# Kernel optimization log

Measured on AMD Instinct MI355X. Metric: run time of the kernel, lower is better.

The kernel has to match this reference:

```python
import jax, jax.numpy as jnp
import numpy as np


def _skew(vec):
    # 3x3 skew-symmetric matrix of a 3-vector
    z = jnp.zeros((), dtype=vec.dtype)
    return jnp.array([[z, -vec[2], vec[1]],
                      [vec[2], z, -vec[0]],
                      [-vec[1], vec[0], z]])


def _exp_se3(w, v, theta):
    W = _skew(w)                      # 3x3
    W2 = W @ W
    s, c = jnp.sin(theta), jnp.cos(theta)
    I3 = jnp.eye(3, dtype=w.dtype)
    R = I3 + s * W + (1.0 - c) * W2                       # rotation block
    V = I3 * theta + (1.0 - c) * W + (theta - s) * W2     # left Jacobian-like
    t = V @ v                                              # translation
    top = jnp.concatenate([R, t[:, None]], axis=1)         # 3x4
    bottom = jnp.array([[0.0, 0.0, 0.0, 1.0]], dtype=w.dtype)
    return jnp.concatenate([top, bottom], axis=0)          # 4x4


def setup_inputs() -> dict:
    key = jax.random.key(0)
    k1, k2, k3, k4 = jax.random.split(key, 4)
    B = 4194304
    return {
        "w": jax.random.normal(k1, (3,), dtype=jnp.float32) * 1e-6,
        "v": jax.random.normal(k2, (3,), dtype=jnp.float32) * 1e-6,
        "theta": jax.random.normal(k3, (), dtype=jnp.float32) * 1e-6,
        "x": jax.random.normal(k4, (B, 4, 4), dtype=jnp.float32),
    }


def reference(w, v, theta, x):
    exp_i = _exp_se3(w, v, theta)              # 4x4
    return jnp.einsum('ij,bjk->bik', exp_i, x)  # broadcast matmul over batch
```

## Files before the change

### kernel.cpp

```cpp
#include <hip/hip_runtime.h>


__global__ __launch_bounds__(256) void se3_apply_kernel(
    const float* __restrict__ w3,
    const float* __restrict__ v3,
    const float* __restrict__ th1,
    const float* __restrict__ x,
    float* __restrict__ out,
    int B)
{
    const float wx = w3[0], wy = w3[1], wz = w3[2];
    const float vx = v3[0], vy = v3[1], vz = v3[2];
    const float th = th1[0];
    const float s = sinf(th);
    const float c = cosf(th);
    const float a = 1.0f - c;
    const float bq = th - s;

    const float W00 = 0.f,  W01 = -wz, W02 =  wy;
    const float W10 =  wz,  W11 = 0.f, W12 = -wx;
    const float W20 = -wy,  W21 =  wx, W22 = 0.f;

    const float Q00 = -(wy*wy + wz*wz), Q01 = wx*wy,            Q02 = wx*wz;
    const float Q10 = wx*wy,            Q11 = -(wx*wx + wz*wz), Q12 = wy*wz;
    const float Q20 = wx*wz,            Q21 = wy*wz,            Q22 = -(wx*wx + wy*wy);

    const float R00 = 1.0f + s*W00 + a*Q00;
    const float R01 =        s*W01 + a*Q01;
    const float R02 =        s*W02 + a*Q02;
    const float R10 =        s*W10 + a*Q10;
    const float R11 = 1.0f + s*W11 + a*Q11;
    const float R12 =        s*W12 + a*Q12;
    const float R20 =        s*W20 + a*Q20;
    const float R21 =        s*W21 + a*Q21;
    const float R22 = 1.0f + s*W22 + a*Q22;

    const float V00 = th   + a*W00 + bq*Q00;
    const float V01 =        a*W01 + bq*Q01;
    const float V02 =        a*W02 + bq*Q02;
    const float V10 =        a*W10 + bq*Q10;
    const float V11 = th   + a*W11 + bq*Q11;
    const float V12 =        a*W12 + bq*Q12;
    const float V20 =        a*W20 + bq*Q20;
    const float V21 =        a*W21 + bq*Q21;
    const float V22 = th   + a*W22 + bq*Q22;

    const float t0 = V00*vx + V01*vy + V02*vz;
    const float t1 = V10*vx + V11*vy + V12*vz;
    const float t2 = V20*vx + V21*vy + V22*vz;

    const int b = blockIdx.x * blockDim.x + threadIdx.x;
    if (b >= B) return;

    const float4* __restrict__ xv = reinterpret_cast<const float4*>(x) + (size_t)b * 4;
    float4* __restrict__ ov       = reinterpret_cast<float4*>(out)      + (size_t)b * 4;

    const float4 r0 = xv[0];
    const float4 r1 = xv[1];
    const float4 r2 = xv[2];
    const float4 r3 = xv[3];

    float4 o0, o1, o2;
    o0.x = R00*r0.x + R01*r1.x + R02*r2.x + t0*r3.x;
    o0.y = R00*r0.y + R01*r1.y + R02*r2.y + t0*r3.y;
    o0.z = R00*r0.z + R01*r1.z + R02*r2.z + t0*r3.z;
    o0.w = R00*r0.w + R01*r1.w + R02*r2.w + t0*r3.w;

    o1.x = R10*r0.x + R11*r1.x + R12*r2.x + t1*r3.x;
    o1.y = R10*r0.y + R11*r1.y + R12*r2.y + t1*r3.y;
    o1.z = R10*r0.z + R11*r1.z + R12*r2.z + t1*r3.z;
    o1.w = R10*r0.w + R11*r1.w + R12*r2.w + t1*r3.w;

    o2.x = R20*r0.x + R21*r1.x + R22*r2.x + t2*r3.x;
    o2.y = R20*r0.y + R21*r1.y + R22*r2.y + t2*r3.y;
    o2.z = R20*r0.z + R21*r1.z + R22*r2.z + t2*r3.z;
    o2.w = R20*r0.w + R21*r1.w + R22*r2.w + t2*r3.w;

    ov[0] = o0;
    ov[1] = o1;
    ov[2] = o2;
    ov[3] = r3;
}

extern "C" void kernel_launch(void* const* d_in, const int* in_sizes, int n_in,
                              void* d_out, int out_size, void* d_ws, size_t ws_size,
                              hipStream_t stream) {
    const float* w  = (const float*)d_in[0];
    const float* v  = (const float*)d_in[1];
    const float* th = (const float*)d_in[2];
    const float* x  = (const float*)d_in[3];
    float* out = (float*)d_out;

    const int B = in_sizes[3] / 16;
    const int block = 256;
    const int grid = (B + block - 1) / block;
    se3_apply_kernel<<<grid, block, 0, stream>>>(w, v, th, x, out, B);
}
```

Before: 448.4 us.

## Assign one output row per thread with cross-lane shuffles for matrix rows

Switches from one 4x4 matrix per thread (four strided float4 loads and stores) to one float4 row per thread, so consecutive lanes access consecutive 16-byte chunks and memory accesses are fully coalesced. Each thread gathers the four rows of its matrix from its 4-lane cluster via 16 shuffles and computes one output row with per-lane selected coefficients. This adds shuffle (LDS crossbar) traffic and launches four times as many threads, each recomputing the exp-map constants.

```diff
diff --git a/kernel.cpp b/kernel.cpp
--- a/kernel.cpp
+++ b/kernel.cpp
@@ -1,13 +1,13 @@
 #include <hip/hip_runtime.h>
 
 
-__global__ __launch_bounds__(256) void se3_apply_kernel(
+__global__ __launch_bounds__(256) void se3_apply_rows(
     const float* __restrict__ w3,
     const float* __restrict__ v3,
     const float* __restrict__ th1,
     const float* __restrict__ x,
     float* __restrict__ out,
-    int B)
+    int NR)
 {
     const float wx = w3[0], wy = w3[1], wz = w3[2];
     const float vx = v3[0], vy = v3[1], vz = v3[2];
@@ -17,69 +17,69 @@
     const float a = 1.0f - c;
     const float bq = th - s;
 
-    const float W00 = 0.f,  W01 = -wz, W02 =  wy;
-    const float W10 =  wz,  W11 = 0.f, W12 = -wx;
-    const float W20 = -wy,  W21 =  wx, W22 = 0.f;
+    const float W01 = -wz, W02 =  wy;
+    const float W10 =  wz, W12 = -wx;
+    const float W20 = -wy, W21 =  wx;
 
     const float Q00 = -(wy*wy + wz*wz), Q01 = wx*wy,            Q02 = wx*wz;
     const float Q10 = wx*wy,            Q11 = -(wx*wx + wz*wz), Q12 = wy*wz;
     const float Q20 = wx*wz,            Q21 = wy*wz,            Q22 = -(wx*wx + wy*wy);
 
-    const float R00 = 1.0f + s*W00 + a*Q00;
+    const float R00 = 1.0f + a*Q00;
     const float R01 =        s*W01 + a*Q01;
     const float R02 =        s*W02 + a*Q02;
     const float R10 =        s*W10 + a*Q10;
-    const float R11 = 1.0f + s*W11 + a*Q11;
+    const float R11 = 1.0f + a*Q11;
     const float R12 =        s*W12 + a*Q12;
     const float R20 =        s*W20 + a*Q20;
     const float R21 =        s*W21 + a*Q21;
-    const float R22 = 1.0f + s*W22 + a*Q22;
+    const float R22 = 1.0f + a*Q22;
 
-    const float V00 = th   + a*W00 + bq*Q00;
+    const float V00 = th   + bq*Q00;
     const float V01 =        a*W01 + bq*Q01;
     const float V02 =        a*W02 + bq*Q02;
     const float V10 =        a*W10 + bq*Q10;
-    const float V11 = th   + a*W11 + bq*Q11;
+    const float V11 = th   + bq*Q11;
     const float V12 =        a*W12 + bq*Q12;
     const float V20 =        a*W20 + bq*Q20;
     const float V21 =        a*W21 + bq*Q21;
-    const float V22 = th   + a*W22 + bq*Q22;
+    const float V22 = th   + bq*Q22;
 
     const float t0 = V00*vx + V01*vy + V02*vz;
     const float t1 = V10*vx + V11*vy + V12*vz;
     const float t2 = V20*vx + V21*vy + V22*vz;
 
-    const int b = blockIdx.x * blockDim.x + threadIdx.x;
-    if (b >= B) return;
+    const int g = blockIdx.x * 256 + threadIdx.x;
+    if (g >= NR) return;
 
-    const float4* __restrict__ xv = reinterpret_cast<const float4*>(x) + (size_t)b * 4;
-    float4* __restrict__ ov       = reinterpret_cast<float4*>(out)      + (size_t)b * 4;
+    const int lane = threadIdx.x & 63;
+    const int i = lane & 3;
+    const int cluster = lane & ~3;
 
-    const float4 r0 = xv[0];
-    const float4 r1 = xv[1];
-    const float4 r2 = xv[2];
-    const float4 r3 = xv[3];
+    const float c0 = (i == 0) ? R00 : (i == 1) ? R10 : (i == 2) ? R20 : 0.0f;
+    const float c1 = (i == 0) ? R01 : (i == 1) ? R11 : (i == 2) ? R21 : 0.0f;
+    const float c2 = (i == 0) ? R02 : (i == 1) ? R12 : (i == 2) ? R22 : 0.0f;
+    const float c3 = (i == 0) ? t0  : (i == 1) ? t1  : (i == 2) ? t2  : 1.0f;
 
-    float4 o0, o1, o2;
-    o0.x = R00*r0.x + R01*r1.x + R02*r2.x + t0*r3.x;
-    o0.y = R00*r0.y + R01*r1.y + R02*r2.y + t0*r3.y;
-    o0.z = R00*r0.z + R01*r1.z + R02*r2.z + t0*r3.z;
-    o0.w = R00*r0.w + R01*r1.w + R02*r2.w + t0*r3.w;
+    const float4 r = reinterpret_cast<const float4*>(x)[g];
 
-    o1.x = R10*r0.x + R11*r1.x + R12*r2.x + t1*r3.x;
-    o1.y = R10*r0.y + R11*r1.y + R12*r2.y + t1*r3.y;
-    o1.z = R10*r0.z + R11*r1.z + R12*r2.z + t1*r3.z;
-    o1.w = R10*r0.w + R11*r1.w + R12*r2.w + t1*r3.w;
+    float4 q0, q1, q2, q3;
+    q0.x = __shfl(r.x, cluster + 0); q0.y = __shfl(r.y, cluster + 0);
+    q0.z = __shfl(r.z, cluster + 0); q0.w = __shfl(r.w, cluster + 0);
+    q1.x = __shfl(r.x, cluster + 1); q1.y = __shfl(r.y, cluster + 1);
+    q1.z = __shfl(r.z, cluster + 1); q1.w = __shfl(r.w, cluster + 1);
+    q2.x = __shfl(r.x, cluster + 2); q2.y = __shfl(r.y, cluster + 2);
+    q2.z = __shfl(r.z, cluster + 2); q2.w = __shfl(r.w, cluster + 2);
+    q3.x = __shfl(r.x, cluster + 3); q3.y = __shfl(r.y, cluster + 3);
+    q3.z = __shfl(r.z, cluster + 3); q3.w = __shfl(r.w, cluster + 3);
 
-    o2.x = R20*r0.x + R21*r1.x + R22*r2.x + t2*r3.x;
-    o2.y = R20*r0.y + R21*r1.y + R22*r2.y + t2*r3.y;
-    o2.z = R20*r0.z + R21*r1.z + R22*r2.z + t2*r3.z;
-    o2.w = R20*r0.w + R21*r1.w + R22*r2.w + t2*r3.w;
+    float4 o;
+    o.x = c0*q0.x + c1*q1.x + c2*q2.x + c3*q3.x;
+    o.y = c0*q0.y + c1*q1.y + c2*q2.y + c3*q3.y;
+    o.z = c0*q0.z + c1*q1.z + c2*q2.z + c3*q3.z;
+    o.w = c0*q0.w + c1*q1.w + c2*q2.w + c3*q3.w;
 
-    ov[0] = o0;
-    ov[1] = o1;
-    ov[2] = o2;
-    ov[3] = r3;
+    reinterpret_cast<float4*>(out)[g] = o;
 }
 
 extern "C" void kernel_launch(void* const* d_in, const int* in_sizes, int n_in,
@@ -91,8 +91,8 @@
     const float* x  = (const float*)d_in[3];
     float* out = (float*)d_out;
 
-    const int B = in_sizes[3] / 16;
+    const int NR = in_sizes[3] / 4;
     const int block = 256;
-    const int grid = (B + block - 1) / block;
-    se3_apply_kernel<<<grid, block, 0, stream>>>(w, v, th, x, out, B);
+    const int grid = (NR + block - 1) / block;
+    se3_apply_rows<<<grid, block, 0, stream>>>(w, v, th, x, out, NR);
 }
```

After: 416.7 us. 1.08x faster.
